# Optimization experiments

Measured on AMD Instinct MI355X. Metric: run time of the kernel, lower is better.

Reference implementation:

```python
import jax, jax.numpy as jnp
import numpy as np


def _cdist(p, t):
    # p: [N,3], t: [N,3] -> euclidean distance matrix [N,N] (torch.cdist p=2)
    d2 = (jnp.sum(p * p, -1)[:, None] + jnp.sum(t * t, -1)[None, :]
          - 2.0 * (p @ t.T))
    return jnp.sqrt(jnp.maximum(d2, 1e-12))


def _greedy_match_cost(cost):
    # cost: [N,N]. For each row i in order, pick the cheapest unused column.
    N = cost.shape[0]

    def step(used, row):
        masked = jnp.where(used, jnp.inf, row)
        j = jnp.argmin(masked)
        c = masked[j]
        return used.at[j].set(True), c

    _, per_point_cost = jax.lax.scan(step, jnp.zeros(N, dtype=bool), cost)
    return jnp.mean(per_point_cost)


def setup_inputs() -> dict:
    key = jax.random.key(0)
    k1, k2 = jax.random.split(key)
    B, N = 8, 2048
    pred = jax.random.normal(k1, (B, N, 3), dtype=jnp.float32)
    target = jax.random.normal(k2, (B, N, 3), dtype=jnp.float32)
    return {"pred": pred, "target": target}


def reference(pred, target):
    # cost matrices per batch: [B,N,N]
    cost = jax.vmap(_cdist)(pred, target)
    emd = jax.vmap(_greedy_match_cost)(cost)  # [B]
    return jnp.mean(emd)
```

## Files before the change

kernel.cpp:

```cpp
#include <hip/hip_runtime.h>

#define NPTS 2048
#define TOPK 32
#define RPB  8
#define MAINBLKS 30
#define TAILROWS (NPTS - MAINBLKS * 64)

typedef float v2f __attribute__((ext_vector_type(2)));
typedef unsigned int u32;
typedef u32 v2u __attribute__((ext_vector_type(2)));
typedef unsigned long long u64;

static __device__ __forceinline__ u32 umin32(u32 a, u32 b) { return b < a ? b : a; }
static __device__ __forceinline__ u64 umin64(u64 a, u64 b) { return b < a ? b : a; }

template <int CTRL>
static __device__ __forceinline__ u32 dpp_min(u32 m) {
  return umin32(m, (u32)__builtin_amdgcn_mov_dpp((int)m, CTRL, 0xF, 0xF, true));
}
static __device__ __forceinline__ u32 x16_min(u32 m) {
#if __has_builtin(__builtin_amdgcn_permlane16_swap)
  auto r = __builtin_amdgcn_permlane16_swap((int)m, (int)m, false, false);
  return umin32(m, umin32((u32)r[0], (u32)r[1]));
#else
  return umin32(m, (u32)__builtin_amdgcn_ds_swizzle((int)m, 0x401F));
#endif
}
static __device__ __forceinline__ u32 x32_min(u32 m) {
#if __has_builtin(__builtin_amdgcn_permlane32_swap)
  auto r = __builtin_amdgcn_permlane32_swap((int)m, (int)m, false, false);
  return umin32(m, umin32((u32)r[0], (u32)r[1]));
#else
  return umin32(m, (u32)__shfl_xor((int)m, 32, 64));
#endif
}
static __device__ __forceinline__ u32 sext_bit(u32 mask, int c) {
#if __has_builtin(__builtin_amdgcn_sbfe)
  return (u32)__builtin_amdgcn_sbfe((int)mask, c, 1);
#else
  return (u32)(((int)(mask << (31 - c))) >> 31);
#endif
}

template <int CTRL>
static __device__ __forceinline__ u64 dpp_min64(u64 k) {
  unsigned lo = (unsigned)k, hi = (unsigned)(k >> 32);
  unsigned olo = (unsigned)__builtin_amdgcn_mov_dpp((int)lo, CTRL, 0xF, 0xF, true);
  unsigned ohi = (unsigned)__builtin_amdgcn_mov_dpp((int)hi, CTRL, 0xF, 0xF, true);
  return umin64(k, ((u64)ohi << 32) | olo);
}
static __device__ __forceinline__ u64 x16_min64(u64 k) {
  unsigned lo = (unsigned)k, hi = (unsigned)(k >> 32);
#if __has_builtin(__builtin_amdgcn_permlane16_swap)
  auto rlo = __builtin_amdgcn_permlane16_swap(lo, lo, false, false);
  auto rhi = __builtin_amdgcn_permlane16_swap(hi, hi, false, false);
  u64 a = ((u64)rhi[0] << 32) | rlo[0];
  u64 b = ((u64)rhi[1] << 32) | rlo[1];
  return umin64(k, umin64(a, b));
#else
  unsigned olo = (unsigned)__builtin_amdgcn_ds_swizzle((int)lo, 0x401F);
  unsigned ohi = (unsigned)__builtin_amdgcn_ds_swizzle((int)hi, 0x401F);
  return umin64(k, ((u64)ohi << 32) | olo);
#endif
}
static __device__ __forceinline__ u64 x32_min64(u64 k) {
  unsigned lo = (unsigned)k, hi = (unsigned)(k >> 32);
#if __has_builtin(__builtin_amdgcn_permlane32_swap)
  auto rlo = __builtin_amdgcn_permlane32_swap(lo, lo, false, false);
  auto rhi = __builtin_amdgcn_permlane32_swap(hi, hi, false, false);
  u64 a = ((u64)rhi[0] << 32) | rlo[0];
  u64 b = ((u64)rhi[1] << 32) | rlo[1];
  return umin64(k, umin64(a, b));
#else
  unsigned olo = (unsigned)__shfl_xor((int)lo, 32, 64);
  unsigned ohi = (unsigned)__shfl_xor((int)hi, 32, 64);
  return umin64(k, ((u64)ohi << 32) | olo);
#endif
}
static __device__ __forceinline__ u64 wave_min_u64(u64 k) {
  k = dpp_min64<0xB1>(k);
  k = dpp_min64<0x4E>(k);
  k = dpp_min64<0x141>(k);
  k = dpp_min64<0x140>(k);
  k = x16_min64(k);
  k = x32_min64(k);
  return k;
}

#define FOR16(M) M(0) M(1) M(2) M(3) M(4) M(5) M(6) M(7) \
                 M(8) M(9) M(10) M(11) M(12) M(13) M(14) M(15)

#define LOADP(h) \
  v2f TX##h, TY##h, TZ##h, TQ##h; \
  { float x0 = tb[6*h+0], y0 = tb[6*h+1], z0 = tb[6*h+2]; \
    float x1 = tb[6*h+3], y1 = tb[6*h+4], z1 = tb[6*h+5]; \
    TX##h = (v2f){x0, x1}; TY##h = (v2f){y0, y1}; TZ##h = (v2f){z0, z1}; \
    TQ##h = (v2f){x0*x0 + y0*y0 + z0*z0, x1*x1 + y1*y1 + z1*z1}; }

#define DISTK(h) u64 KA##h, KB##h; { \
  v2f dot = __builtin_elementwise_fma(TX##h, Xv, \
              __builtin_elementwise_fma(TY##h, Yv, TZ##h * Zv)); \
  v2f dd  = __builtin_elementwise_fma(m2v, dot, TQ##h); \
  v2f d2  = Qv + dd; \
  float c0 = fmaxf(d2.x, 1e-12f), c1 = fmaxf(d2.y, 1e-12f); \
  KA##h = ((u64)(u32)__float_as_int(c0) << 32) | (u32)(base + 2*(h)); \
  KB##h = ((u64)(u32)__float_as_int(c1) << 32) | (u32)(base + 2*(h) + 1); }

#define G4(a, b, c, d) umin64(umin64(a, b), umin64(c, d))
#define ZG(c, KV, RL) case (c): KV = own ? ~0ULL : KV; goto RL;

__global__ __launch_bounds__(64, 2) void emd_topk_kernel(
    const float* __restrict__ pred, const float* __restrict__ target,
    u64* __restrict__ lists) {
  const int blk = blockIdx.x;
  const int b  = blk / (NPTS / RPB);
  const int r0 = (blk % (NPTS / RPB)) * RPB;
  const int lane = threadIdx.x;
  const float* p = pred + (size_t)b * NPTS * 3;
  const float* t = target + (size_t)b * NPTS * 3;

  const float* tb = t + (size_t)lane * 32 * 3;
  FOR16(LOADP)
  const int base = lane << 5;
  const v2f m2v = {-2.f, -2.f};

#pragma unroll 1
  for (int rr = 0; rr < RPB; ++rr) {
    const int i = r0 + rr;
    const float X = p[3 * i], Y = p[3 * i + 1], Z = p[3 * i + 2];
    const float Q = fmaf(X, X, fmaf(Y, Y, Z * Z));
    const v2f Xv = {X, X}, Yv = {Y, Y}, Zv = {Z, Z}, Qv = {Q, Q};
    FOR16(DISTK)

    u64 g0 = G4(KA0, KB0, KA1, KB1),   g1 = G4(KA2, KB2, KA3, KB3);
    u64 g2 = G4(KA4, KB4, KA5, KB5),   g3 = G4(KA6, KB6, KA7, KB7);
    u64 g4 = G4(KA8, KB8, KA9, KB9),   g5 = G4(KA10, KB10, KA11, KB11);
    u64 g6 = G4(KA12, KB12, KA13, KB13), g7 = G4(KA14, KB14, KA15, KB15);
    u64 h0 = umin64(g0, g1), h1 = umin64(g2, g3);
    u64 h2 = umin64(g4, g5), h3 = umin64(g6, g7);
    u64 q0 = umin64(h0, h1), q1 = umin64(h2, h3);
    u64 root = umin64(q0, q1);

    u64* out = lists + ((size_t)b * NPTS + i) * TOPK;
#pragma unroll 1
    for (int e = 0; e < TOPK; ++e) {
      u64 m = wave_min_u64(root);
      if (lane == 0) out[e] = m;
      if (e == TOPK - 1) break;
      const u32 col = (u32)m & (u32)(NPTS - 1);
      const bool own = (lane == (int)(col >> 5));
      const u32 k5 = col & 31u;
      switch (k5) {
        ZG(0,  KA0,  R0) ZG(1,  KB0,  R0) ZG(2,  KA1,  R0) ZG(3,  KB1,  R0)
        ZG(4,  KA2,  R1) ZG(5,  KB2,  R1) ZG(6,  KA3,  R1) ZG(7,  KB3,  R1)
        ZG(8,  KA4,  R2) ZG(9,  KB4,  R2) ZG(10, KA5,  R2) ZG(11, KB5,  R2)
        ZG(12, KA6,  R3) ZG(13, KB6,  R3) ZG(14, KA7,  R3) ZG(15, KB7,  R3)
        ZG(16, KA8,  R4) ZG(17, KB8,  R4) ZG(18, KA9,  R4) ZG(19, KB9,  R4)
        ZG(20, KA10, R5) ZG(21, KB10, R5) ZG(22, KA11, R5) ZG(23, KB11, R5)
        ZG(24, KA12, R6) ZG(25, KB12, R6) ZG(26, KA13, R6) ZG(27, KB13, R6)
        ZG(28, KA14, R7) ZG(29, KB14, R7) ZG(30, KA15, R7) ZG(31, KB15, R7)
        default: __builtin_unreachable();
      }
      R0: g0 = G4(KA0, KB0, KA1, KB1);     h0 = umin64(g0, g1); q0 = umin64(h0, h1); root = umin64(q0, q1); continue;
      R1: g1 = G4(KA2, KB2, KA3, KB3);     h0 = umin64(g0, g1); q0 = umin64(h0, h1); root = umin64(q0, q1); continue;
      R2: g2 = G4(KA4, KB4, KA5, KB5);     h1 = umin64(g2, g3); q0 = umin64(h0, h1); root = umin64(q0, q1); continue;
      R3: g3 = G4(KA6, KB6, KA7, KB7);     h1 = umin64(g2, g3); q0 = umin64(h0, h1); root = umin64(q0, q1); continue;
      R4: g4 = G4(KA8, KB8, KA9, KB9);     h2 = umin64(g4, g5); q1 = umin64(h2, h3); root = umin64(q0, q1); continue;
      R5: g5 = G4(KA10, KB10, KA11, KB11); h2 = umin64(g4, g5); q1 = umin64(h2, h3); root = umin64(q0, q1); continue;
      R6: g6 = G4(KA12, KB12, KA13, KB13); h3 = umin64(g6, g7); q1 = umin64(h2, h3); root = umin64(q0, q1); continue;
      R7: g7 = G4(KA14, KB14, KA15, KB15); h3 = umin64(g6, g7); q1 = umin64(h2, h3); root = umin64(q0, q1); continue;
    }
  }
}


#define LD16(M) M(0) M(1) M(2) M(3) M(4) M(5) M(6) M(7) \
                M(8) M(9) M(10) M(11) M(12) M(13) M(14) M(15)
#define DECLA(j) uint4 A##j;
#define LDA(j)   A##j = Lr[j];
#define WRC(j)   { cl64w[(2*(j)) * 64 + lane]     = ((u64)A##j.y << 32) | A##j.x; \
                   cl64w[(2*(j) + 1) * 64 + lane] = ((u64)A##j.w << 32) | A##j.z; }
#define FREEB(j) { \
    u32 c0 = A##j.x & 2047u, c1 = A##j.z & 2047u; \
    u32 w0 = sbm[c0 >> 5], w1 = sbm[c1 >> 5]; \
    alive |= ((~(w0 >> (c0 & 31u))) & 1u) << (2*(j)); \
    alive |= ((~(w1 >> (c1 & 31u))) & 1u) << (2*(j)+1); }

#define CASCADE() { \
    int guard_ = 0; \
    while (true) { \
      bool changed_ = false; \
      if (!committed && !exh) { \
        int g2_ = 0; \
        while (true) { \
          u32 c_ = vclaim[col]; \
          if (c_ >= (u32)lane) break; \
          alive &= ~(1u << rank); \
          if (alive == 0u) { exh = true; break; } \
          rank = (u32)__ffs(alive) - 1u; \
          cur = cl64[rank * 64 + lane]; \
          col = (u32)cur & 2047u; \
          atomicMin(&claim[col], (u32)lane); \
          changed_ = true; \
          if (++g2_ > 33) break; \
        } \
      } \
      if (__ballot(changed_) == 0ULL) break; \
      if (++guard_ > 3000) break; \
    } }

__global__ __launch_bounds__(64, 1) void emd_seq_kernel(
    const float* __restrict__ pred, const float* __restrict__ target,
    const u64* __restrict__ lists, float* __restrict__ batch_sums) {
  const int b = blockIdx.x, lane = threadIdx.x;
  const float* t = target + (size_t)b * NPTS * 3;
  const float* p = pred + (size_t)b * NPTS * 3;

  __shared__ float4 tt[NPTS];
  __shared__ u64 cl64s[TOPK * 64];
  __shared__ u32 claim[NPTS];
  __shared__ u32 fl[NPTS];
  __shared__ u32 sbitmap[64];
  __shared__ float4 ppred[64];
  __shared__ float4 tpred[TAILROWS];

  for (int j = lane; j < NPTS; j += 64) {
    float x = t[3 * j], y = t[3 * j + 1], z = t[3 * j + 2];
    tt[((j & 31) << 6) | ((j >> 5) ^ (j & 31))] =
        make_float4(x, y, z, fmaf(x, x, fmaf(y, y, z * z)));
  }
  sbitmap[lane] = 0u;
  __syncthreads();

  const u64* L = lists + (size_t)b * NPTS * TOPK;
  u64* cl64w = cl64s;
  const u64* cl64 = cl64s;
  volatile u32* sbm = sbitmap;
  volatile u32* vclaim = claim;
  float psum = 0.f;

  const uint4* Lr = (const uint4*)(L + (size_t)lane * TOPK);
  LD16(DECLA)
  LD16(LDA)

#pragma unroll 1
  for (int blk = 0; blk < MAINBLKS; ++blk) {
    LD16(WRC)
    u32 alive = 0u;
    LD16(FREEB)
    { const float* pr = p + (size_t)(blk * 64 + lane) * 3;
      float X = pr[0], Y = pr[1], Z = pr[2];
      ppred[lane] = make_float4(X, Y, Z, fmaf(X, X, fmaf(Y, Y, Z * Z))); }
    { int nrow = (blk + 1) * 64 + lane; nrow = nrow < NPTS ? nrow : NPTS - 1;
      Lr = (const uint4*)(L + (size_t)nrow * TOPK); }
    LD16(LDA)
#pragma unroll
    for (int k = 0; k < 32; ++k) claim[k * 64 + lane] = ~0u;

    bool committed = false;
    bool exh = (alive == 0u);
    u32 rank = 0, col = 0;
    u64 cur = 0;
    if (!exh) {
      rank = (u32)__ffs(alive) - 1u;
      cur = cl64[rank * 64 + lane];
      col = (u32)cur & 2047u;
      atomicMin(&claim[col], (u32)lane);
    }
    CASCADE()

    bool flBuilt = false;
    u32 F = 0;
    int oguard = 0;
#pragma unroll 1
    while (true) {
      u64 exbl = __ballot(exh && !committed);
      if (exbl == 0ULL) break;
      int rstar = __ffsll(exbl) - 1;

      if (!committed && !exh && lane < rstar) {
        atomicOr(&sbitmap[col >> 5], 1u << (col & 31u));
        psum += sqrtf(__uint_as_float((u32)(cur >> 32)));
        committed = true;
      }

      if (!flBuilt) {
        u32 fw = ~sbm[lane];
        u32 cnt = __popc(fw);
        u32 pfx = cnt;
#pragma unroll
        for (int d = 1; d < 64; d <<= 1) {
          u32 o = (u32)__shfl_up((int)pfx, d, 64);
          if (lane >= d) pfx += o;
        }
        F = (u32)__shfl((int)pfx, 63, 64);
        pfx -= cnt;
        while (fw) {
          int bpos = __ffs(fw) - 1;
          fw &= fw - 1u;
          fl[pfx++] = ((u32)lane << 5) + (u32)bpos;
        }
        flBuilt = true;
      }

      u32 cst;
      {
        float4 P4 = ppred[rstar];
        float X = P4.x, Y = P4.y, Z = P4.z, Q = P4.w;
        u64 mb = ~0ULL;
        for (u32 k = (u32)lane; k < F; k += 64) {
          u32 c = fl[k];
          u32 used = (sbm[c >> 5] >> (c & 31u)) & 1u;
          float4 c4 = tt[((c & 31u) << 6) | ((c >> 5) ^ (c & 31u))];
          float dot = fmaf(c4.x, X, fmaf(c4.y, Y, c4.z * Z));
          float d2 = Q + fmaf(-2.f, dot, c4.w);
          d2 = fmaxf(d2, 1e-12f);
          u64 kk = ((u64)(u32)__float_as_int(d2) << 32) | c;
          if (used) kk = ~0ULL;
          mb = umin64(mb, kk);
        }
        mb = wave_min_u64(mb);
        cst = (u32)mb & 2047u;
        if (lane == rstar) {
          psum += sqrtf(__uint_as_float((u32)(mb >> 32)));
          committed = true;
        }
      }
      u32 prev = vclaim[cst];
      if (lane == rstar) {
        atomicOr(&sbitmap[cst >> 5], 1u << (cst & 31u));
        atomicMin(&claim[cst], (u32)rstar);
      }
      if (prev != ~0u) {
        CASCADE()
      }
      if (++oguard > 80) break;
    }

    if (!committed) {
      atomicOr(&sbitmap[col >> 5], 1u << (col & 31u));
      psum += sqrtf(__uint_as_float((u32)(cur >> 32)));
    }
  }

  {
    u32 fw = ~sbm[lane];
    u32 cnt = __popc(fw);
    u32 pfx = cnt;
#pragma unroll
    for (int d = 1; d < 64; d <<= 1) {
      u32 o = (u32)__shfl_up((int)pfx, d, 64);
      if (lane >= d) pfx += o;
    }
    u32 F = (u32)__shfl((int)pfx, 63, 64);
    pfx -= cnt;
    while (fw) {
      int bpos = __ffs(fw) - 1;
      fw &= fw - 1u;
      fl[pfx++] = ((u32)lane << 5) + (u32)bpos;
    }
    { const float* pr = p + (size_t)(MAINBLKS * 64 + lane) * 3;
      float X = pr[0], Y = pr[1], Z = pr[2];
      tpred[lane] = make_float4(X, Y, Z, fmaf(X, X, fmaf(Y, Y, Z * Z))); }
    { const float* pr = p + (size_t)(MAINBLKS * 64 + 64 + lane) * 3;
      float X = pr[0], Y = pr[1], Z = pr[2];
      tpred[64 + lane] = make_float4(X, Y, Z, fmaf(X, X, fmaf(Y, Y, Z * Z))); }

    bool l0 = (u32)lane < F, l1 = (u32)(64 + lane) < F;
    u32 c0 = l0 ? fl[lane] : 0u;
    u32 c1 = l1 ? fl[64 + lane] : 0u;
    float4 t0 = tt[((c0 & 31u) << 6) | ((c0 >> 5) ^ (c0 & 31u))];
    float4 t1 = tt[((c1 & 31u) << 6) | ((c1 >> 5) ^ (c1 & 31u))];

#pragma unroll 1
    for (int r = 0; r < TAILROWS; ++r) {
      float4 P = tpred[r];
      float X = P.x, Y = P.y, Z = P.z, Q = P.w;
      float dot0 = fmaf(t0.x, X, fmaf(t0.y, Y, t0.z * Z));
      float d20 = fmaxf(Q + fmaf(-2.f, dot0, t0.w), 1e-12f);
      float dot1 = fmaf(t1.x, X, fmaf(t1.y, Y, t1.z * Z));
      float d21 = fmaxf(Q + fmaf(-2.f, dot1, t1.w), 1e-12f);
      u64 k0 = l0 ? (((u64)(u32)__float_as_int(d20) << 32) | c0) : ~0ULL;
      u64 k1 = l1 ? (((u64)(u32)__float_as_int(d21) << 32) | c1) : ~0ULL;
      u64 k = wave_min_u64(umin64(k0, k1));
      u32 wc = (u32)k & 2047u;
      l0 = l0 && (c0 != wc);
      l1 = l1 && (c1 != wc);
      if (lane == 0) psum += sqrtf(__uint_as_float((u32)(k >> 32)));
    }
  }

  float v = psum;
  v += __shfl_xor(v, 1, 64);
  v += __shfl_xor(v, 2, 64);
  v += __shfl_xor(v, 4, 64);
  v += __shfl_xor(v, 8, 64);
  v += __shfl_xor(v, 16, 64);
  v += __shfl_xor(v, 32, 64);
  if (lane == 0) batch_sums[b] = v;
}

#define DECLRU(h) v2u RU##h;
#define DIST(h) { \
  v2f dot = __builtin_elementwise_fma(TX##h, Xv, \
              __builtin_elementwise_fma(TY##h, Yv, TZ##h * Zv)); \
  v2f dd  = __builtin_elementwise_fma(m2v, dot, TQ##h); \
  v2f d2  = Qv + dd; \
  RU##h = (v2u){(u32)__float_as_int(d2.x), (u32)__float_as_int(d2.y)}; }
#define TOUR(h, c) { \
  u32 u0 = RU##h.x | sext_bit(usedmask, 2*h); \
  u32 u1 = RU##h.y | sext_bit(usedmask, 2*h + 1); \
  u32 pu = umin32(u0, u1); \
  u32 pk = (u1 < u0) ? (u32)(2*h + 1) : (u32)(2*h); \
  if (pu < bc##c) { bc##c = pu; kc##c = pk; } }

__global__ __launch_bounds__(64, 1) void emd_greedy_kernel(
    const float* __restrict__ pred, const float* __restrict__ target,
    float* __restrict__ batch_sums) {
  const int b = blockIdx.x, lane = threadIdx.x;
  const float* p = pred + (size_t)b * NPTS * 3;
  const float* t = target + (size_t)b * NPTS * 3;
  __shared__ float4 pp[NPTS + 2];
  for (int i = lane; i < NPTS; i += 64) {
    float x = p[3 * i], y = p[3 * i + 1], z = p[3 * i + 2];
    pp[i] = make_float4(x, y, z, x * x + y * y + z * z);
  }
  if (lane < 2) pp[NPTS + lane] = make_float4(0.f, 0.f, 0.f, 0.f);
  const float* tb = t + (size_t)lane * 32 * 3;
  FOR16(LOADP)
  FOR16(DECLRU)
  u32 usedmask = 0;
  float sum = 0.f;
  __syncthreads();
  const v2f m2v = {-2.f, -2.f};
  v2f Xv, Yv, Zv, Qv;
  {
    float4 A = pp[0];
    Xv = (v2f){A.x, A.x}; Yv = (v2f){A.y, A.y};
    Zv = (v2f){A.z, A.z}; Qv = (v2f){A.w, A.w};
    FOR16(DIST)
  }
  for (int i = 0; i < NPTS; ++i) {
    float4 An = pp[i + 1];
    u32 bc0 = ~0u, bc1 = ~0u, bc2 = ~0u, bc3 = ~0u;
    u32 kc0 = 0, kc1 = 0, kc2 = 0, kc3 = 0;
    TOUR(0, 0)  TOUR(1, 0)  TOUR(2, 0)  TOUR(3, 0)
    TOUR(4, 1)  TOUR(5, 1)  TOUR(6, 1)  TOUR(7, 1)
    TOUR(8, 2)  TOUR(9, 2)  TOUR(10, 2) TOUR(11, 2)
    TOUR(12, 3) TOUR(13, 3) TOUR(14, 3) TOUR(15, 3)
    bool s01 = bc1 < bc0; u32 v01 = s01 ? bc1 : bc0; u32 i01 = s01 ? kc1 : kc0;
    bool s23 = bc3 < bc2; u32 v23 = s23 ? bc3 : bc2; u32 i23 = s23 ? kc3 : kc2;
    bool sf  = v23 < v01; u32 bu  = sf ? v23 : v01; u32 bk  = sf ? i23 : i01;
    Xv = (v2f){An.x, An.x}; Yv = (v2f){An.y, An.y};
    Zv = (v2f){An.z, An.z}; Qv = (v2f){An.w, An.w};
    FOR16(DIST)
    u32 m = bu;
    m = dpp_min<0xB1>(m); m = dpp_min<0x4E>(m);
    m = dpp_min<0x141>(m); m = dpp_min<0x140>(m);
    m = x16_min(m); m = x32_min(m);
    u64 mk = __ballot(bu == m);
    int first = __ffsll(mk) - 1;
    usedmask |= (lane == first) ? (1u << bk) : 0u;
    sum += sqrtf(fmaxf(__uint_as_float(m), 1e-12f));
  }
  if (lane == 0) batch_sums[b] = sum;
}

__global__ void emd_finalize_kernel(const float* __restrict__ batch_sums,
                                    float* __restrict__ out, int B) {
  float acc = 0.f;
  for (int b = 0; b < B; ++b) acc += batch_sums[b] / (float)NPTS;
  out[0] = acc / (float)B;
}

extern "C" void kernel_launch(void* const* d_in, const int* in_sizes, int n_in,
                              void* d_out, int out_size, void* d_ws, size_t ws_size,
                              hipStream_t stream) {
  const float* pred   = (const float*)d_in[0];
  const float* target = (const float*)d_in[1];
  float* out = (float*)d_out;
  const int B = in_sizes[0] / (NPTS * 3);

  const size_t need = 256 + (size_t)B * NPTS * TOPK * sizeof(u64);
  if (ws_size >= need) {
    float* bs = (float*)d_ws;
    u64* lists = (u64*)((char*)d_ws + 256);
    emd_topk_kernel<<<B * (NPTS / RPB), 64, 0, stream>>>(pred, target, lists);
    emd_seq_kernel<<<B, 64, 0, stream>>>(pred, target, lists, bs);
    emd_finalize_kernel<<<1, 1, 0, stream>>>(bs, out, B);
  } else {
    float* bs = (float*)d_ws;
    emd_greedy_kernel<<<B, 64, 0, stream>>>(pred, target, bs);
    emd_finalize_kernel<<<1, 1, 0, stream>>>(bs, out, B);
  }
}
```

Before: 395.8 us.

## Warp-specialize sequential EMD kernel with producer waves double-buffering next block

The sequential greedy-matching kernel now runs with four waves instead of one. Wave 0 does the serial matching. Waves 1-3 prefetch and stage the next block's top-k candidate lists, reset its claim array, and load its pred rows into double-buffered shared memory. The goal is to take the global-load latency and claim-array reset off the serial critical path. In exchange it adds a __syncthreads per block and doubles the shared buffers, and the consumer now reads the alive mask from shared memory instead of registers.

```diff
diff --git a/kernel.cpp b/kernel.cpp
--- a/kernel.cpp
+++ b/kernel.cpp
@@ -178,13 +178,8 @@
                 M(8) M(9) M(10) M(11) M(12) M(13) M(14) M(15)
 #define DECLA(j) uint4 A##j;
 #define LDA(j)   A##j = Lr[j];
-#define WRC(j)   { cl64w[(2*(j)) * 64 + lane]     = ((u64)A##j.y << 32) | A##j.x; \
-                   cl64w[(2*(j) + 1) * 64 + lane] = ((u64)A##j.w << 32) | A##j.z; }
-#define FREEB(j) { \
-    u32 c0 = A##j.x & 2047u, c1 = A##j.z & 2047u; \
-    u32 w0 = sbm[c0 >> 5], w1 = sbm[c1 >> 5]; \
-    alive |= ((~(w0 >> (c0 & 31u))) & 1u) << (2*(j)); \
-    alive |= ((~(w1 >> (c1 & 31u))) & 1u) << (2*(j)+1); }
+#define WRCD(j)  { dst[(2*(j)) * 64 + lane]     = ((u64)A##j.y << 32) | A##j.x; \
+                   dst[(2*(j) + 1) * 64 + lane] = ((u64)A##j.w << 32) | A##j.z; }
 
 #define CASCADE() { \
     int guard_ = 0; \
@@ -198,9 +193,9 @@
           alive &= ~(1u << rank); \
           if (alive == 0u) { exh = true; break; } \
           rank = (u32)__ffs(alive) - 1u; \
-          cur = cl64[rank * 64 + lane]; \
+          cur = cl[rank * 64 + lane]; \
           col = (u32)cur & 2047u; \
-          atomicMin(&claim[col], (u32)lane); \
+          atomicMin(&claimCur[col], (u32)lane); \
           changed_ = true; \
           if (++g2_ > 33) break; \
         } \
@@ -209,141 +204,188 @@
       if (++guard_ > 3000) break; \
     } }
 
-__global__ __launch_bounds__(64, 1) void emd_seq_kernel(
+__global__ __launch_bounds__(256, 1) void emd_seq_kernel(
     const float* __restrict__ pred, const float* __restrict__ target,
     const u64* __restrict__ lists, float* __restrict__ batch_sums) {
-  const int b = blockIdx.x, lane = threadIdx.x;
+  const int b = blockIdx.x;
+  const int tid = threadIdx.x;
+  const int w = tid >> 6, lane = tid & 63;
   const float* t = target + (size_t)b * NPTS * 3;
   const float* p = pred + (size_t)b * NPTS * 3;
 
   __shared__ float4 tt[NPTS];
-  __shared__ u64 cl64s[TOPK * 64];
-  __shared__ u32 claim[NPTS];
+  __shared__ u64 cl64s[2][TOPK * 64];
+  __shared__ u32 claimb[2][NPTS];
   __shared__ u32 fl[NPTS];
   __shared__ u32 sbitmap[64];
-  __shared__ float4 ppred[64];
+  __shared__ float4 ppredb[2][64];
   __shared__ float4 tpred[TAILROWS];
 
-  for (int j = lane; j < NPTS; j += 64) {
+  for (int j = tid; j < NPTS; j += 256) {
     float x = t[3 * j], y = t[3 * j + 1], z = t[3 * j + 2];
     tt[((j & 31) << 6) | ((j >> 5) ^ (j & 31))] =
         make_float4(x, y, z, fmaf(x, x, fmaf(y, y, z * z)));
   }
-  sbitmap[lane] = 0u;
-  __syncthreads();
+  if (tid < 64) sbitmap[tid] = 0u;
 
   const u64* L = lists + (size_t)b * NPTS * TOPK;
-  u64* cl64w = cl64s;
-  const u64* cl64 = cl64s;
   volatile u32* sbm = sbitmap;
-  volatile u32* vclaim = claim;
   float psum = 0.f;
 
-  const uint4* Lr = (const uint4*)(L + (size_t)lane * TOPK);
+  const uint4* Lr;
   LD16(DECLA)
-  LD16(LDA)
+
+  if (w == 1) {
+    Lr = (const uint4*)(L + (size_t)lane * TOPK);
+    LD16(LDA)
+    u64* dst = &cl64s[0][0];
+    LD16(WRCD)
+    Lr = (const uint4*)(L + (size_t)(64 + lane) * TOPK);
+    LD16(LDA)
+  } else if (w == 2) {
+#pragma unroll
+    for (int k = 0; k < 32; ++k) claimb[0][k * 64 + lane] = ~0u;
+  } else if (w == 3) {
+    { const float* pr = p + (size_t)lane * 3;
+      float X = pr[0], Y = pr[1], Z = pr[2];
+      ppredb[0][lane] = make_float4(X, Y, Z, fmaf(X, X, fmaf(Y, Y, Z * Z))); }
+    { const float* pr = p + (size_t)(MAINBLKS * 64 + lane) * 3;
+      float X = pr[0], Y = pr[1], Z = pr[2];
+      tpred[lane] = make_float4(X, Y, Z, fmaf(X, X, fmaf(Y, Y, Z * Z))); }
+    { const float* pr = p + (size_t)(MAINBLKS * 64 + 64 + lane) * 3;
+      float X = pr[0], Y = pr[1], Z = pr[2];
+      tpred[64 + lane] = make_float4(X, Y, Z, fmaf(X, X, fmaf(Y, Y, Z * Z))); }
+  }
 
 #pragma unroll 1
   for (int blk = 0; blk < MAINBLKS; ++blk) {
-    LD16(WRC)
-    u32 alive = 0u;
-    LD16(FREEB)
-    { const float* pr = p + (size_t)(blk * 64 + lane) * 3;
-      float X = pr[0], Y = pr[1], Z = pr[2];
-      ppred[lane] = make_float4(X, Y, Z, fmaf(X, X, fmaf(Y, Y, Z * Z))); }
-    { int nrow = (blk + 1) * 64 + lane; nrow = nrow < NPTS ? nrow : NPTS - 1;
-      Lr = (const uint4*)(L + (size_t)nrow * TOPK); }
-    LD16(LDA)
+    __syncthreads();
+
+    if (w == 1) {
+      if (blk + 1 < MAINBLKS) {
+        u64* dst = &cl64s[(blk + 1) & 1][0];
+        LD16(WRCD)
+        if (blk + 2 < MAINBLKS) {
+          Lr = (const uint4*)(L + (size_t)((blk + 2) * 64 + lane) * TOPK);
+          LD16(LDA)
+        }
+      }
+    } else if (w == 2) {
+      if (blk + 1 < MAINBLKS) {
 #pragma unroll
-    for (int k = 0; k < 32; ++k) claim[k * 64 + lane] = ~0u;
-
-    bool committed = false;
-    bool exh = (alive == 0u);
-    u32 rank = 0, col = 0;
-    u64 cur = 0;
-    if (!exh) {
-      rank = (u32)__ffs(alive) - 1u;
-      cur = cl64[rank * 64 + lane];
-      col = (u32)cur & 2047u;
-      atomicMin(&claim[col], (u32)lane);
-    }
-    CASCADE()
-
-    bool flBuilt = false;
-    u32 F = 0;
-    int oguard = 0;
+        for (int k = 0; k < 32; ++k) claimb[(blk + 1) & 1][k * 64 + lane] = ~0u;
+      }
+    } else if (w == 3) {
+      if (blk + 1 < MAINBLKS) {
+        const float* pr = p + (size_t)((blk + 1) * 64 + lane) * 3;
+        float X = pr[0], Y = pr[1], Z = pr[2];
+        ppredb[(blk + 1) & 1][lane] =
+            make_float4(X, Y, Z, fmaf(X, X, fmaf(Y, Y, Z * Z)));
+      }
+    } else {
+      const u64* cl = &cl64s[blk & 1][0];
+      u32* claimCur = &claimb[blk & 1][0];
+      volatile u32* vclaim = claimCur;
+      const float4* ppcur = &ppredb[blk & 1][0];
+
+      u32 alive = 0u;
+#pragma unroll
+      for (int j = 0; j < 32; ++j) {
+        u32 c = (u32)cl[j * 64 + lane] & 2047u;
+        u32 wd = sbm[c >> 5];
+        alive |= ((~(wd >> (c & 31u))) & 1u) << j;
+      }
+
+      bool committed = false;
+      bool exh = (alive == 0u);
+      u32 rank = 0, col = 0;
+      u64 cur = 0;
+      if (!exh) {
+        rank = (u32)__ffs(alive) - 1u;
+        cur = cl[rank * 64 + lane];
+        col = (u32)cur & 2047u;
+        atomicMin(&claimCur[col], (u32)lane);
+      }
+      CASCADE()
+
+      bool flBuilt = false;
+      u32 F = 0;
+      int oguard = 0;
 #pragma unroll 1
-    while (true) {
-      u64 exbl = __ballot(exh && !committed);
-      if (exbl == 0ULL) break;
-      int rstar = __ffsll(exbl) - 1;
-
-      if (!committed && !exh && lane < rstar) {
+      while (true) {
+        u64 exbl = __ballot(exh && !committed);
+        if (exbl == 0ULL) break;
+        int rstar = __ffsll(exbl) - 1;
+
+        if (!committed && !exh && lane < rstar) {
+          atomicOr(&sbitmap[col >> 5], 1u << (col & 31u));
+          psum += sqrtf(__uint_as_float((u32)(cur >> 32)));
+          committed = true;
+        }
+
+        if (!flBuilt) {
+          u32 fw = ~sbm[lane];
+          u32 cnt = __popc(fw);
+          u32 pfx = cnt;
+#pragma unroll
+          for (int d = 1; d < 64; d <<= 1) {
+            u32 o = (u32)__shfl_up((int)pfx, d, 64);
+            if (lane >= d) pfx += o;
+          }
+          F = (u32)__shfl((int)pfx, 63, 64);
+          pfx -= cnt;
+          while (fw) {
+            int bpos = __ffs(fw) - 1;
+            fw &= fw - 1u;
+            fl[pfx++] = ((u32)lane << 5) + (u32)bpos;
+          }
+          flBuilt = true;
+        }
+
+        u32 cst;
+        {
+          float4 P4 = ppcur[rstar];
+          float X = P4.x, Y = P4.y, Z = P4.z, Q = P4.w;
+          u64 mb = ~0ULL;
+          for (u32 k = (u32)lane; k < F; k += 64) {
+            u32 c = fl[k];
+            u32 used = (sbm[c >> 5] >> (c & 31u)) & 1u;
+            float4 c4 = tt[((c & 31u) << 6) | ((c >> 5) ^ (c & 31u))];
+            float dot = fmaf(c4.x, X, fmaf(c4.y, Y, c4.z * Z));
+            float d2 = Q + fmaf(-2.f, dot, c4.w);
+            d2 = fmaxf(d2, 1e-12f);
+            u64 kk = ((u64)(u32)__float_as_int(d2) << 32) | c;
+            if (used) kk = ~0ULL;
+            mb = umin64(mb, kk);
+          }
+          mb = wave_min_u64(mb);
+          cst = (u32)mb & 2047u;
+          if (lane == rstar) {
+            psum += sqrtf(__uint_as_float((u32)(mb >> 32)));
+            committed = true;
+          }
+        }
+        u32 prev = vclaim[cst];
+        if (lane == rstar) {
+          atomicOr(&sbitmap[cst >> 5], 1u << (cst & 31u));
+          atomicMin(&claimCur[cst], (u32)rstar);
+        }
+        if (prev != ~0u) {
+          CASCADE()
+        }
+        if (++oguard > 80) break;
+      }
+
+      if (!committed) {
         atomicOr(&sbitmap[col >> 5], 1u << (col & 31u));
         psum += sqrtf(__uint_as_float((u32)(cur >> 32)));
-        committed = true;
-      }
-
-      if (!flBuilt) {
-        u32 fw = ~sbm[lane];
-        u32 cnt = __popc(fw);
-        u32 pfx = cnt;
-#pragma unroll
-        for (int d = 1; d < 64; d <<= 1) {
-          u32 o = (u32)__shfl_up((int)pfx, d, 64);
-          if (lane >= d) pfx += o;
-        }
-        F = (u32)__shfl((int)pfx, 63, 64);
-        pfx -= cnt;
-        while (fw) {
-          int bpos = __ffs(fw) - 1;
-          fw &= fw - 1u;
-          fl[pfx++] = ((u32)lane << 5) + (u32)bpos;
-        }
-        flBuilt = true;
-      }
-
-      u32 cst;
-      {
-        float4 P4 = ppred[rstar];
-        float X = P4.x, Y = P4.y, Z = P4.z, Q = P4.w;
-        u64 mb = ~0ULL;
-        for (u32 k = (u32)lane; k < F; k += 64) {
-          u32 c = fl[k];
-          u32 used = (sbm[c >> 5] >> (c & 31u)) & 1u;
-          float4 c4 = tt[((c & 31u) << 6) | ((c >> 5) ^ (c & 31u))];
-          float dot = fmaf(c4.x, X, fmaf(c4.y, Y, c4.z * Z));
-          float d2 = Q + fmaf(-2.f, dot, c4.w);
-          d2 = fmaxf(d2, 1e-12f);
-          u64 kk = ((u64)(u32)__float_as_int(d2) << 32) | c;
-          if (used) kk = ~0ULL;
-          mb = umin64(mb, kk);
-        }
-        mb = wave_min_u64(mb);
-        cst = (u32)mb & 2047u;
-        if (lane == rstar) {
-          psum += sqrtf(__uint_as_float((u32)(mb >> 32)));
-          committed = true;
-        }
-      }
-      u32 prev = vclaim[cst];
-      if (lane == rstar) {
-        atomicOr(&sbitmap[cst >> 5], 1u << (cst & 31u));
-        atomicMin(&claim[cst], (u32)rstar);
-      }
-      if (prev != ~0u) {
-        CASCADE()
-      }
-      if (++oguard > 80) break;
+      }
     }
-
-    if (!committed) {
-      atomicOr(&sbitmap[col >> 5], 1u << (col & 31u));
-      psum += sqrtf(__uint_as_float((u32)(cur >> 32)));
-    }
-  }
-
-  {
+  }
+
+  __syncthreads();
+
+  if (w == 0) {
     u32 fw = ~sbm[lane];
     u32 cnt = __popc(fw);
     u32 pfx = cnt;
@@ -359,12 +401,6 @@
       fw &= fw - 1u;
       fl[pfx++] = ((u32)lane << 5) + (u32)bpos;
     }
-    { const float* pr = p + (size_t)(MAINBLKS * 64 + lane) * 3;
-      float X = pr[0], Y = pr[1], Z = pr[2];
-      tpred[lane] = make_float4(X, Y, Z, fmaf(X, X, fmaf(Y, Y, Z * Z))); }
-    { const float* pr = p + (size_t)(MAINBLKS * 64 + 64 + lane) * 3;
-      float X = pr[0], Y = pr[1], Z = pr[2];
-      tpred[64 + lane] = make_float4(X, Y, Z, fmaf(X, X, fmaf(Y, Y, Z * Z))); }
 
     bool l0 = (u32)lane < F, l1 = (u32)(64 + lane) < F;
     u32 c0 = l0 ? fl[lane] : 0u;
@@ -388,16 +424,16 @@
       l1 = l1 && (c1 != wc);
       if (lane == 0) psum += sqrtf(__uint_as_float((u32)(k >> 32)));
     }
-  }
-
-  float v = psum;
-  v += __shfl_xor(v, 1, 64);
-  v += __shfl_xor(v, 2, 64);
-  v += __shfl_xor(v, 4, 64);
-  v += __shfl_xor(v, 8, 64);
-  v += __shfl_xor(v, 16, 64);
-  v += __shfl_xor(v, 32, 64);
-  if (lane == 0) batch_sums[b] = v;
+
+    float v = psum;
+    v += __shfl_xor(v, 1, 64);
+    v += __shfl_xor(v, 2, 64);
+    v += __shfl_xor(v, 4, 64);
+    v += __shfl_xor(v, 8, 64);
+    v += __shfl_xor(v, 16, 64);
+    v += __shfl_xor(v, 32, 64);
+    if (lane == 0) batch_sums[b] = v;
+  }
 }
 
 #define DECLRU(h) v2u RU##h;
@@ -486,7 +522,7 @@
     float* bs = (float*)d_ws;
     u64* lists = (u64*)((char*)d_ws + 256);
     emd_topk_kernel<<<B * (NPTS / RPB), 64, 0, stream>>>(pred, target, lists);
-    emd_seq_kernel<<<B, 64, 0, stream>>>(pred, target, lists, bs);
+    emd_seq_kernel<<<B, 256, 0, stream>>>(pred, target, lists, bs);
     emd_finalize_kernel<<<1, 1, 0, stream>>>(bs, out, B);
   } else {
     float* bs = (float*)d_ws;
```

Result: no change. 397.6 us (+0.5%).
